# Optimization experiments

Hardware: AMD Instinct MI355X
Metric: run time of the kernel (lower is better)

The kernel has to match this reference:

```python
import jax, jax.numpy as jnp
import numpy as np

B, T, H, D = 256, 128, 256, 256
N_SUB = 2  # fixed-step RK4 substeps per observation interval (replaces adaptive odeint)


def setup_inputs() -> dict:
    key = jax.random.key(0)
    ks = jax.random.split(key, 16)
    # timestamps: strictly increasing, shared across batch (torch code uses b[0,:,0])
    times = jnp.cumsum(jax.random.uniform(ks[0], (T,), minval=0.05, maxval=0.15)) + 0.1
    vals = jax.random.uniform(ks[1], (B, T))
    b = jnp.stack([jnp.broadcast_to(times, (B, T)), vals], axis=-1)  # (B,T,2)
    u = jax.random.uniform(ks[2], (B, T))
    train_m = (u < 0.4).astype(jnp.float32)
    test_m = ((u >= 0.4) & (u < 0.7)).astype(jnp.float32)
    m = train_m + test_m  # disjoint -> in {0,1}
    h0 = jnp.zeros((B, H), jnp.float32)
    s = 0.05
    p = lambda k, shp: jax.random.normal(k, shp, jnp.float32) * s
    return {
        'b': b, 'm': m, 'train_m': train_m, 'test_m': test_m, 'h0': h0,
        # ODE func: Linear(H->D) then Linear(D->H) then tanh
        'W1': p(ks[3], (D, H)), 'b1': p(ks[4], (D,)),
        'W2': p(ks[5], (H, D)), 'b2': p(ks[6], (H,)),
        # GRUCell(input_size=1, hidden=H), torch layout (3H, in)
        'W_ih': p(ks[7], (3 * H, 1)), 'W_hh': p(ks[8], (3 * H, H)),
        'b_ih': p(ks[9], (3 * H,)), 'b_hh': p(ks[10], (3 * H,)),
        # output heads: Linear(H->D), Linear(D->1), tanh
        'Wo1': p(ks[11], (D, H)), 'bo1': p(ks[12], (D,)),
        'Wo2': p(ks[13], (1, D)), 'bo2': p(ks[14], (1,)),
    }


def _gru(x, h, W_ih, W_hh, b_ih, b_hh):
    gi = x @ W_ih.T + b_ih          # (B, 3H)
    gh = h @ W_hh.T + b_hh          # (B, 3H)
    i_r, i_z, i_n = jnp.split(gi, 3, axis=-1)
    h_r, h_z, h_n = jnp.split(gh, 3, axis=-1)
    r = jax.nn.sigmoid(i_r + h_r)
    z = jax.nn.sigmoid(i_z + h_z)
    n = jnp.tanh(i_n + r * h_n)
    return (1.0 - z) * n + z * h


def _ode_rnn(b, m, train_m, test_m, h0, W1, b1, W2, b2,
             W_ih, W_hh, b_ih, b_hh, Wo1, bo1, Wo2, bo2):
    f = lambda x: jnp.tanh((x @ W1.T + b1) @ W2.T + b2)  # autonomous ODE func

    def rk4(h, t0, t1):
        dt = (t1 - t0) / N_SUB
        def sub(h, _):
            k1 = f(h)
            k2 = f(h + 0.5 * dt * k1)
            k3 = f(h + 0.5 * dt * k2)
            k4 = f(h + dt * k3)
            return h + (dt / 6.0) * (k1 + 2.0 * k2 + 2.0 * k3 + k4), None
        h, _ = jax.lax.scan(sub, h, None, length=N_SUB)
        return h

    times = b[0, :, 0]                                      # (T,)
    t0s = jnp.concatenate([jnp.zeros((1,), times.dtype), times[:-1]])
    vals = b[:, :, 1]                                       # (B,T)

    def step(h, inp):
        t0, t1, bv, mv, trm, tem = inp
        hp = rk4(h, t0, t1)                                 # (B,H)
        out = jnp.tanh((hp @ Wo1.T + bo1) @ Wo2.T + bo2)[:, 0]  # (B,)
        htrain = _gru((bv * trm)[:, None], hp, W_ih, W_hh, b_ih, b_hh)
        htest = _gru((out * tem)[:, None], hp, W_ih, W_hh, b_ih, b_hh)
        h_new = trm[:, None] * htrain + tem[:, None] * htest + (1.0 - mv)[:, None] * hp
        return h_new, out

    xs = (t0s, times, vals.T, m.T, train_m.T, test_m.T)
    _, outs = jax.lax.scan(step, h0, xs)                    # outs: (T,B)
    return outs.T                                           # (B,T)


def reference(b, m, train_m, test_m, h0, W1, b1, W2, b2,
              W_ih, W_hh, b_ih, b_hh, Wo1, bo1, Wo2, bo2):
    return _ode_rnn(b, m, train_m, test_m, h0, W1, b1, W2, b2,
                    W_ih, W_hh, b_ih, b_hh, Wo1, bo1, Wo2, bo2)
```

## Files before the change

### kernel.cpp

```cpp
#include <hip/hip_runtime.h>

#define H 256
#define T_STEPS 128
#define B_BATCH 256
#define XPAD 68
#define I_LDS 44

__device__ __forceinline__ float sigmoidf_(float x) { return 1.0f / (1.0f + expf(-x)); }


__global__ void prep_weff(const float* __restrict__ W1, const float* __restrict__ W2,
                          const float* __restrict__ b1, const float* __restrict__ b2,
                          float* __restrict__ Weff, float* __restrict__ beff) {
    int i = blockIdx.x, j = threadIdx.x;
    const float* w2row = W2 + j * H;
    float acc = 0.f;
    for (int d = 0; d < H; ++d) acc += W1[d * H + i] * w2row[d];
    Weff[i * H + j] = acc;
    if (i == 0) {
        float bacc = b2[j];
        for (int d = 0; d < H; ++d) bacc += b1[d] * w2row[d];
        beff[j] = bacc;
    }
}

__global__ void prep_whht(const float* __restrict__ Whh, float* __restrict__ WhhT) {
    int idx = blockIdx.x * blockDim.x + threadIdx.x;
    int i = idx / 768;
    int r = idx - i * 768;
    WhhT[idx] = Whh[r * H + i];
}

__global__ void prep_wo(const float* __restrict__ Wo1, const float* __restrict__ Wo2,
                        const float* __restrict__ bo1, const float* __restrict__ bo2,
                        float* __restrict__ wo, float* __restrict__ bo) {
    int i = threadIdx.x;
    float acc = 0.f;
    for (int d = 0; d < H; ++d) acc += Wo1[d * H + i] * Wo2[d];
    wo[i] = acc;
    float p = bo1[i] * Wo2[i];
    __shared__ float red[4];
    for (int off = 32; off > 0; off >>= 1) p += __shfl_down(p, off);
    if ((i & 63) == 0) red[i >> 6] = p;
    __syncthreads();
    if (i == 0) bo[0] = red[0] + red[1] + red[2] + red[3] + bo2[0];
}


__global__ __attribute__((amdgpu_flat_work_group_size(1024, 1024),
                          amdgpu_waves_per_eu(4, 4)))
void ode_rnn_main(
    const float* __restrict__ b_in, const float* __restrict__ m_in,
    const float* __restrict__ trm_in, const float* __restrict__ tem_in,
    const float* __restrict__ h0,
    const float* __restrict__ Weff, const float* __restrict__ beff,
    const float* __restrict__ WhhT,
    const float* __restrict__ W_ih, const float* __restrict__ b_ih,
    const float* __restrict__ b_hh,
    const float* __restrict__ wo, const float* __restrict__ bo_p,
    float* __restrict__ out)
{
    const int tid = threadIdx.x;
    const int bb  = blockIdx.x;
    const int j   = tid >> 2;
    const int q   = tid & 3;

    __shared__ float whh_lds[I_LDS * 768];
    __shared__ __align__(16) float xsb[2][4 * XPAD];
    __shared__ __align__(16) float xsf[H];
    __shared__ float gh_lds[768];
    __shared__ float red[4];
    __shared__ float times_s[T_STEPS];
    __shared__ float bv_s[T_STEPS], trm_s[T_STEPS], tem_s[T_STEPS], m_s[T_STEPS];

    float wreg[64];
    #pragma unroll
    for (int p = 0; p < 64; ++p) wreg[p] = Weff[(q * 64 + p) * H + j];
    #pragma unroll
    for (int p = 0; p < 64; ++p) asm volatile("" : "+v"(wreg[p]));

    for (int k = tid; k < I_LDS * 768; k += 1024) whh_lds[k] = WhhT[k];

    if (tid < T_STEPS) {
        times_s[tid] = b_in[2 * tid];
        int bt = bb * T_STEPS + tid;
        bv_s[tid]  = b_in[2 * bt + 1];
        trm_s[tid] = trm_in[bt];
        tem_s[tid] = tem_in[bt];
        m_s[tid]   = m_in[bt];
    }

    float h = h0[bb * H + j];
    const float be   = beff[j];
    const float bihr = b_ih[j], bihz = b_ih[H + j], bihn = b_ih[2 * H + j];
    const float bhhr = b_hh[j], bhhz = b_hh[H + j], bhhn = b_hh[2 * H + j];
    const float wihr = W_ih[j], wihz = W_ih[H + j], wihn = W_ih[2 * H + j];
    const float bo   = bo_p[0];
    const float wo_t = (tid >= 768) ? wo[tid - 768] : 0.f;

    const int myidx = j + 4 * (j >> 6);

    if (q == 0) xsb[0][myidx] = h;
    __syncthreads();

    #define EVAL(KOUT) do {                                        \
        const float* xp_ = &xsb[cur][q * XPAD];                    \
        float a0_ = 0.f, a1_ = 0.f, a2_ = 0.f, a3_ = 0.f;          \
        _Pragma("unroll")                                          \
        for (int p = 0; p < 64; p += 8) {                          \
            float4 xa_ = *(const float4*)(xp_ + p);                \
            float4 xb_ = *(const float4*)(xp_ + p + 4);            \
            a0_ = fmaf(xa_.x, wreg[p + 0], a0_);                   \
            a1_ = fmaf(xa_.y, wreg[p + 1], a1_);                   \
            a2_ = fmaf(xa_.z, wreg[p + 2], a2_);                   \
            a3_ = fmaf(xa_.w, wreg[p + 3], a3_);                   \
            a0_ = fmaf(xb_.x, wreg[p + 4], a0_);                   \
            a1_ = fmaf(xb_.y, wreg[p + 5], a1_);                   \
            a2_ = fmaf(xb_.z, wreg[p + 6], a2_);                   \
            a3_ = fmaf(xb_.w, wreg[p + 7], a3_);                   \
        }                                                          \
        float s_ = (a0_ + a1_) + (a2_ + a3_);                      \
        s_ += __shfl_xor(s_, 1);                                   \
        s_ += __shfl_xor(s_, 2);                                   \
        KOUT = tanhf(be + s_);                                     \
    } while (0)

    #define PUBLISH(V) do {                                        \
        if (q == 0) xsb[cur ^ 1][myidx] = (V);                     \
        __syncthreads();                                           \
        cur ^= 1;                                                  \
    } while (0)

    float tprev = 0.f;
    for (int t = 0; t < T_STEPS; ++t) {
        float t1 = times_s[t];
        float dt = (t1 - tprev) * 0.5f;
        tprev = t1;

        int cur = 0;
        float k1, k2, k3, k4;
        #pragma unroll 1
        for (int s = 0; s < 2; ++s) {
            EVAL(k1); PUBLISH(fmaf(0.5f * dt, k1, h));
            EVAL(k2); PUBLISH(fmaf(0.5f * dt, k2, h));
            EVAL(k3); PUBLISH(fmaf(dt, k3, h));
            EVAL(k4);
            h = fmaf(dt * (1.f / 6.f), k1 + 2.f * (k2 + k3) + k4, h);
            if (s == 0) PUBLISH(h);
        }

        if (q == 0) xsf[j] = h;
        __syncthreads();

        if (tid < 768) {
            float g0 = 0.f, g1 = 0.f, g2 = 0.f, g3 = 0.f;
            const float* wl = whh_lds + tid;
            #pragma unroll 4
            for (int i = 0; i < I_LDS; i += 4) {
                float4 xv = *(const float4*)(xsf + i);
                g0 = fmaf(xv.x, wl[(i + 0) * 768], g0);
                g1 = fmaf(xv.y, wl[(i + 1) * 768], g1);
                g2 = fmaf(xv.z, wl[(i + 2) * 768], g2);
                g3 = fmaf(xv.w, wl[(i + 3) * 768], g3);
            }
            const float* wr = WhhT + I_LDS * 768 + tid;
            #pragma unroll 8
            for (int i = 0; i < H - I_LDS; i += 4) {
                float4 xv = *(const float4*)(xsf + I_LDS + i);
                g0 = fmaf(xv.x, wr[(i + 0) * 768], g0);
                g1 = fmaf(xv.y, wr[(i + 1) * 768], g1);
                g2 = fmaf(xv.z, wr[(i + 2) * 768], g2);
                g3 = fmaf(xv.w, wr[(i + 3) * 768], g3);
            }
            gh_lds[tid] = (g0 + g1) + (g2 + g3);
        } else {
            float p = xsf[tid - 768] * wo_t;
            #pragma unroll
            for (int off = 32; off > 0; off >>= 1) p += __shfl_down(p, off);
            if ((tid & 63) == 0) red[(tid - 768) >> 6] = p;
        }
        __syncthreads();

        {
            float outv = tanhf(red[0] + red[1] + red[2] + red[3] + bo);
            float bv = bv_s[t], trm = trm_s[t], tem = tem_s[t], mv = m_s[t];
            float ghr = gh_lds[j] + bhhr;
            float ghz = gh_lds[256 + j] + bhhz;
            float ghn = gh_lds[512 + j] + bhhn;
            float x1v = bv * trm, x2v = outv * tem;

            float r1 = sigmoidf_(fmaf(x1v, wihr, bihr) + ghr);
            float z1 = sigmoidf_(fmaf(x1v, wihz, bihz) + ghz);
            float n1 = tanhf(fmaf(x1v, wihn, bihn) + r1 * ghn);
            float h1 = (1.f - z1) * n1 + z1 * h;

            float r2 = sigmoidf_(fmaf(x2v, wihr, bihr) + ghr);
            float z2 = sigmoidf_(fmaf(x2v, wihz, bihz) + ghz);
            float n2 = tanhf(fmaf(x2v, wihn, bihn) + r2 * ghn);
            float h2 = (1.f - z2) * n2 + z2 * h;

            if (tid == 0) out[bb * T_STEPS + t] = outv;
            h = trm * h1 + tem * h2 + (1.f - mv) * h;
        }

        if (q == 0) xsb[0][myidx] = h;
        __syncthreads();
    }
    #undef EVAL
    #undef PUBLISH
}


extern "C" void kernel_launch(void* const* d_in, const int* in_sizes, int n_in,
                              void* d_out, int out_size, void* d_ws, size_t ws_size,
                              hipStream_t stream) {
    const float* b_in = (const float*)d_in[0];
    const float* m_in = (const float*)d_in[1];
    const float* trm  = (const float*)d_in[2];
    const float* tem  = (const float*)d_in[3];
    const float* h0   = (const float*)d_in[4];
    const float* W1   = (const float*)d_in[5];
    const float* b1   = (const float*)d_in[6];
    const float* W2   = (const float*)d_in[7];
    const float* b2   = (const float*)d_in[8];
    const float* W_ih = (const float*)d_in[9];
    const float* W_hh = (const float*)d_in[10];
    const float* b_ih = (const float*)d_in[11];
    const float* b_hh = (const float*)d_in[12];
    const float* Wo1  = (const float*)d_in[13];
    const float* bo1  = (const float*)d_in[14];
    const float* Wo2  = (const float*)d_in[15];
    const float* bo2  = (const float*)d_in[16];

    float* ws   = (float*)d_ws;
    float* Weff = ws;
    float* beff = Weff + 65536;
    float* WhhT = beff + 256;
    float* wo   = WhhT + 196608;
    float* bo   = wo + 256;

    prep_weff<<<256, 256, 0, stream>>>(W1, W2, b1, b2, Weff, beff);
    prep_whht<<<192, 1024, 0, stream>>>(W_hh, WhhT);
    prep_wo<<<1, 256, 0, stream>>>(Wo1, Wo2, bo1, bo2, wo, bo);

    ode_rnn_main<<<B_BATCH, 1024, 0, stream>>>(b_in, m_in, trm, tem, h0,
                                               Weff, beff, WhhT,
                                               W_ih, b_ih, b_hh, wo, bo,
                                               (float*)d_out);
}
```

Before: 2.287 ms.

## Split ODE matvec over 8 lanes with two outputs per thread pair

The register-resident Weff matvec changes from 4 lanes per output (64 weights each) to 8 lanes each holding 32 input rows for two adjacent output columns, loaded as float2. Each LDS float4 load of x now feeds eight FMAs instead of four, cutting LDS traffic per FMA, at the cost of a 3-step shuffle reduction on two values. The state publish layout is regrouped into 8 padded groups, and I_LDS rises to 48 so more of W_hh sits in shared memory and less is read from global memory each step. Lanes with the same c duplicate the GRU math for their column, and the pragma unroll 1 on the time loop keeps code size down.

```diff
diff --git a/kernel.cpp b/kernel.cpp
--- a/kernel.cpp
+++ b/kernel.cpp
@@ -3,8 +3,8 @@
 #define H 256
 #define T_STEPS 128
 #define B_BATCH 256
-#define XPAD 68
-#define I_LDS 44
+#define I_LDS 48
+#define XGRP 36
 
 __device__ __forceinline__ float sigmoidf_(float x) { return 1.0f / (1.0f + expf(-x)); }
 
@@ -62,25 +62,28 @@
 {
     const int tid = threadIdx.x;
     const int bb  = blockIdx.x;
-    const int j   = tid >> 2;
-    const int q   = tid & 3;
+    const int jp  = tid >> 3;
+    const int e   = tid & 7;
+    const int c   = e & 1;
+    const int jc  = 2 * jp + c;
 
     __shared__ float whh_lds[I_LDS * 768];
-    __shared__ __align__(16) float xsb[2][4 * XPAD];
+    __shared__ __align__(16) float xsb[2][8 * XGRP];
     __shared__ __align__(16) float xsf[H];
     __shared__ float gh_lds[768];
     __shared__ float red[4];
     __shared__ float times_s[T_STEPS];
     __shared__ float bv_s[T_STEPS], trm_s[T_STEPS], tem_s[T_STEPS], m_s[T_STEPS];
 
-    float wreg[64];
+    float2 wregv[32];
     #pragma unroll
-    for (int p = 0; p < 64; ++p) wreg[p] = Weff[(q * 64 + p) * H + j];
+    for (int il = 0; il < 32; ++il)
+        wregv[il] = *(const float2*)&Weff[(32 * e + il) * H + 2 * jp];
     #pragma unroll
-    for (int p = 0; p < 64; ++p) asm volatile("" : "+v"(wreg[p]));
+    for (int il = 0; il < 32; ++il)
+        asm volatile("" : "+v"(wregv[il].x), "+v"(wregv[il].y));
 
     for (int k = tid; k < I_LDS * 768; k += 1024) whh_lds[k] = WhhT[k];
-
     if (tid < T_STEPS) {
         times_s[tid] = b_in[2 * tid];
         int bt = bb * T_STEPS + tid;
@@ -90,48 +93,51 @@
         m_s[tid]   = m_in[bt];
     }
 
-    float h = h0[bb * H + j];
-    const float be   = beff[j];
-    const float bihr = b_ih[j], bihz = b_ih[H + j], bihn = b_ih[2 * H + j];
-    const float bhhr = b_hh[j], bhhz = b_hh[H + j], bhhn = b_hh[2 * H + j];
-    const float wihr = W_ih[j], wihz = W_ih[H + j], wihn = W_ih[2 * H + j];
+    float h = h0[bb * H + jc];
+    const float be   = beff[jc];
+    const float bihr = b_ih[jc], bihz = b_ih[H + jc], bihn = b_ih[2 * H + jc];
+    const float bhhr = b_hh[jc], bhhz = b_hh[H + jc], bhhn = b_hh[2 * H + jc];
+    const float wihr = W_ih[jc], wihz = W_ih[H + jc], wihn = W_ih[2 * H + jc];
     const float bo   = bo_p[0];
     const float wo_t = (tid >= 768) ? wo[tid - 768] : 0.f;
 
-    const int myidx = j + 4 * (j >> 6);
-
-    if (q == 0) xsb[0][myidx] = h;
+    const int pubpos = (jc >> 5) * XGRP + (jc & 31);
+
+    if (e < 2) xsb[0][pubpos] = h;
     __syncthreads();
 
-    #define EVAL(KOUT) do {                                        \
-        const float* xp_ = &xsb[cur][q * XPAD];                    \
-        float a0_ = 0.f, a1_ = 0.f, a2_ = 0.f, a3_ = 0.f;          \
+    #define EVAL(KOUT_) do {                                       \
+        const float* xp_ = &xsb[cur][e * XGRP];                    \
+        float a0_ = 0.f, a1_ = 0.f, b0_ = 0.f, b1_ = 0.f;          \
         _Pragma("unroll")                                          \
-        for (int p = 0; p < 64; p += 8) {                          \
-            float4 xa_ = *(const float4*)(xp_ + p);                \
-            float4 xb_ = *(const float4*)(xp_ + p + 4);            \
-            a0_ = fmaf(xa_.x, wreg[p + 0], a0_);                   \
-            a1_ = fmaf(xa_.y, wreg[p + 1], a1_);                   \
-            a2_ = fmaf(xa_.z, wreg[p + 2], a2_);                   \
-            a3_ = fmaf(xa_.w, wreg[p + 3], a3_);                   \
-            a0_ = fmaf(xb_.x, wreg[p + 4], a0_);                   \
-            a1_ = fmaf(xb_.y, wreg[p + 5], a1_);                   \
-            a2_ = fmaf(xb_.z, wreg[p + 6], a2_);                   \
-            a3_ = fmaf(xb_.w, wreg[p + 7], a3_);                   \
+        for (int g_ = 0; g_ < 8; ++g_) {                           \
+            float4 x_ = ((const float4*)xp_)[g_];                  \
+            a0_ = fmaf(x_.x, wregv[4 * g_ + 0].x, a0_);            \
+            b0_ = fmaf(x_.x, wregv[4 * g_ + 0].y, b0_);            \
+            a1_ = fmaf(x_.y, wregv[4 * g_ + 1].x, a1_);            \
+            b1_ = fmaf(x_.y, wregv[4 * g_ + 1].y, b1_);            \
+            a0_ = fmaf(x_.z, wregv[4 * g_ + 2].x, a0_);            \
+            b0_ = fmaf(x_.z, wregv[4 * g_ + 2].y, b0_);            \
+            a1_ = fmaf(x_.w, wregv[4 * g_ + 3].x, a1_);            \
+            b1_ = fmaf(x_.w, wregv[4 * g_ + 3].y, b1_);            \
         }                                                          \
-        float s_ = (a0_ + a1_) + (a2_ + a3_);                      \
-        s_ += __shfl_xor(s_, 1);                                   \
-        s_ += __shfl_xor(s_, 2);                                   \
-        KOUT = tanhf(be + s_);                                     \
+        float s0_ = a0_ + a1_, s1_ = b0_ + b1_;                    \
+        _Pragma("unroll")                                          \
+        for (int o_ = 1; o_ < 8; o_ <<= 1) {                       \
+            s0_ += __shfl_xor(s0_, o_);                            \
+            s1_ += __shfl_xor(s1_, o_);                            \
+        }                                                          \
+        KOUT_ = tanhf(be + (c == 0 ? s0_ : s1_));                  \
     } while (0)
 
-    #define PUBLISH(V) do {                                        \
-        if (q == 0) xsb[cur ^ 1][myidx] = (V);                     \
+    #define PUBLISH(V_) do {                                       \
+        if (e < 2) xsb[cur ^ 1][pubpos] = (V_);                    \
         __syncthreads();                                           \
         cur ^= 1;                                                  \
     } while (0)
 
     float tprev = 0.f;
+    #pragma unroll 1
     for (int t = 0; t < T_STEPS; ++t) {
         float t1 = times_s[t];
         float dt = (t1 - tprev) * 0.5f;
@@ -149,7 +155,7 @@
             if (s == 0) PUBLISH(h);
         }
 
-        if (q == 0) xsf[j] = h;
+        if (e < 2) xsf[jc] = h;
         __syncthreads();
 
         if (tid < 768) {
@@ -184,9 +190,9 @@
         {
             float outv = tanhf(red[0] + red[1] + red[2] + red[3] + bo);
             float bv = bv_s[t], trm = trm_s[t], tem = tem_s[t], mv = m_s[t];
-            float ghr = gh_lds[j] + bhhr;
-            float ghz = gh_lds[256 + j] + bhhz;
-            float ghn = gh_lds[512 + j] + bhhn;
+            float ghr = gh_lds[jc] + bhhr;
+            float ghz = gh_lds[256 + jc] + bhhz;
+            float ghn = gh_lds[512 + jc] + bhhn;
             float x1v = bv * trm, x2v = outv * tem;
 
             float r1 = sigmoidf_(fmaf(x1v, wihr, bihr) + ghr);
@@ -203,7 +209,7 @@
             h = trm * h1 + tem * h2 + (1.f - mv) * h;
         }
 
-        if (q == 0) xsb[0][myidx] = h;
+        if (e < 2) xsb[0][pubpos] = h;
         __syncthreads();
     }
     #undef EVAL
```

Result: faster. 2.169 ms (-5.2%).
